# Kernel tuning notes

Measured on AMD Instinct MI355X. Metric: run time of the kernel, lower is better.

The kernel has to match this reference:

```python
import jax, jax.numpy as jnp
import numpy as np

B, S, IN_DIM, D, H, L, C = 8, 1024, 256, 1024, 16, 6, 10
DK = D // H
EPS = 1e-5


def setup_inputs() -> dict:
    key = jax.random.key(0)
    ks = iter(jax.random.split(key, 64))
    n = lambda shape, s=0.02: jax.random.normal(next(ks), shape, dtype=jnp.float32) * s
    inp = {
        'x': jax.random.normal(next(ks), (B, S, IN_DIM), dtype=jnp.float32),
        'emb_w': n((IN_DIM, D)), 'emb_b': jnp.zeros((D,), jnp.float32),
        'Wq': n((L, D, D)), 'bq': jnp.zeros((L, D), jnp.float32),
        'Wk': n((L, D, D)), 'bk': jnp.zeros((L, D), jnp.float32),
        'Wv': n((L, D, D)), 'bv': jnp.zeros((L, D), jnp.float32),
        'Wo': n((L, D, D)), 'bo': jnp.zeros((L, D), jnp.float32),
        'W1': n((L, D, 4 * D)), 'b1': jnp.zeros((L, 4 * D), jnp.float32),
        'W2': n((L, 4 * D, D)), 'b2': jnp.zeros((L, D), jnp.float32),
        'ln1_s': jnp.ones((L, D), jnp.float32), 'ln1_b': jnp.zeros((L, D), jnp.float32),
        'ln2_s': jnp.ones((L, D), jnp.float32), 'ln2_b': jnp.zeros((L, D), jnp.float32),
        'fc_w': n((D, C)), 'fc_b': jnp.zeros((C,), jnp.float32),
    }
    return inp


def _pos_encoding_rows(n_rows):
    # Faithful to the torch module: pe is [max_len,1,D]; pe[:x.size(0)] picks the
    # first `batch` positions and broadcasts over the sequence dim.
    pos = jnp.arange(n_rows, dtype=jnp.float32)[:, None]
    div = jnp.exp(jnp.arange(0, D, 2, dtype=jnp.float32) * (-np.log(10000.0) / D))
    pe = jnp.zeros((n_rows, D), jnp.float32)
    pe = pe.at[:, 0::2].set(jnp.sin(pos * div)).at[:, 1::2].set(jnp.cos(pos * div))
    return pe


def _layer_norm(x, scale, bias):
    mu = jnp.mean(x, axis=-1, keepdims=True)
    var = jnp.mean(jnp.square(x - mu), axis=-1, keepdims=True)
    return (x - mu) * jax.lax.rsqrt(var + EPS) * scale + bias


def reference(x, emb_w, emb_b, Wq, bq, Wk, bk, Wv, bv, Wo, bo,
              W1, b1, W2, b2, ln1_s, ln1_b, ln2_s, ln2_b, fc_w, fc_b):
    h = x @ emb_w + emb_b                              # [B,S,D]
    h = h + _pos_encoding_rows(B)[:, None, :]          # broadcast pe[:B] over seq
    scale = 1.0 / np.sqrt(DK)
    for i in range(L):
        def heads(y, W, b):
            return (y @ W + b).reshape(B, S, H, DK).transpose(0, 2, 1, 3)  # bhsd
        q = heads(h, Wq[i], bq[i])
        k = heads(h, Wk[i], bk[i])
        v = heads(h, Wv[i], bv[i])
        scores = jnp.einsum('bhqd,bhkd->bhqk', q, k) * scale
        p = jax.nn.softmax(scores, axis=-1)
        o = jnp.einsum('bhqk,bhkd->bhqd', p, v)
        o = o.transpose(0, 2, 1, 3).reshape(B, S, D)
        attn_out = o @ Wo[i] + bo[i]
        h = _layer_norm(h + attn_out, ln1_s[i], ln1_b[i])
        ff = jax.nn.relu(h @ W1[i] + b1[i]) @ W2[i] + b2[i]
        h = _layer_norm(h + ff, ln2_s[i], ln2_b[i])
    pooled = jnp.mean(h, axis=1)                       # [B,D]
    return pooled @ fc_w + fc_b                        # [B,C]
```

## Files before the change

kernel.cpp:

```cpp
#include <hip/hip_runtime.h>
#include <stdint.h>

#define B_   8
#define S_   1024
#define IND  256
#define D_   1024
#define H_   16
#define DKH  64
#define L_   6
#define FF   4096
#define NTOK (B_*S_)

typedef __bf16 bf16;
typedef __attribute__((ext_vector_type(4))) float  f32x4;
typedef __attribute__((ext_vector_type(8))) __bf16 bf16x8;
typedef __attribute__((ext_vector_type(4))) __bf16 bf16x4;
typedef __attribute__((ext_vector_type(2))) __bf16 bf16x2;

#define AS1 __attribute__((address_space(1)))
#define AS3 __attribute__((address_space(3)))

__device__ __forceinline__ void gload16(const void* g, void* l) {
  __builtin_amdgcn_global_load_lds((AS1 void*)(const_cast<void*>(g)), (AS3 void*)l, 16, 0, 0);
}

__global__ __launch_bounds__(256)
void k_trans(const float* __restrict__ in, bf16* __restrict__ out,
             int K, int N, long inStride, long outStride) {
  __shared__ float t[32][33];
  const float* inp = in + (long)blockIdx.z * inStride;
  bf16* outp = out + (long)blockIdx.z * outStride;
  const int n0 = blockIdx.x * 32, k0 = blockIdx.y * 32;
  const int tx = threadIdx.x & 31, ty = threadIdx.x >> 5;
  #pragma unroll
  for (int j = 0; j < 32; j += 8)
    t[ty + j][tx] = inp[(long)(k0 + ty + j) * N + n0 + tx];
  __syncthreads();
  #pragma unroll
  for (int j = 0; j < 32; j += 8)
    outp[(long)(n0 + ty + j) * K + k0 + tx] = (bf16)t[tx][ty + j];
}

__global__ __launch_bounds__(256)
void k_f2b(const float* __restrict__ in, bf16* __restrict__ out) {
  const long i = ((long)blockIdx.x * 256 + threadIdx.x) * 4;
  f32x4 v = *(const f32x4*)(in + i);
  bf16x4 o;
  #pragma unroll
  for (int j = 0; j < 4; ++j) o[j] = (bf16)v[j];
  *(bf16x4*)(out + i) = o;
}

__global__ __launch_bounds__(256)
void k_pe(float* __restrict__ pe) {
  const int i = blockIdx.x * 256 + threadIdx.x;
  const int b = i >> 10, d = i & 1023;
  const float k2 = (float)(d & ~1);
  const float dv = __expf(k2 * (-9.210340371976184f / (float)D_));
  const float a = (float)b * dv;
  pe[i] = (d & 1) ? cosf(a) : sinf(a);
}

__global__ __launch_bounds__(256)
void k_packb(const float* __restrict__ bq, const float* __restrict__ bk,
             const float* __restrict__ bv, float* __restrict__ out) {
  const int i = blockIdx.x * 256 + threadIdx.x;
  const int l = i / 3072, j = i % 3072;
  const float* src = (j < 1024) ? bq : ((j < 2048) ? bk : bv);
  out[i] = src[l * 1024 + (j & 1023)];
}

template<int EPI>
__global__ __launch_bounds__(256)
void k_gemm(const bf16* __restrict__ A, const bf16* __restrict__ Bt,
            const float* __restrict__ bias,
            void* __restrict__ out0, void* __restrict__ out1,
            const float* __restrict__ pe,
            int M, int N, int K) {
  __shared__ __align__(16) bf16 sA[128 * 32];
  __shared__ __align__(16) bf16 sB[128 * 32];
  const int tid = threadIdx.x;
  const int lane = tid & 63, wv = tid >> 6;
  const int bx = blockIdx.x, by = blockIdx.y;
  const int wm = wv >> 1, wn = wv & 1;
  const int lg = lane >> 4, lc = lane & 15;
  const long arow0 = (long)by * 128;
  const long brow0 = (long)bx * 128;
  const int c0 = (wv * 2 + 0) * 64 + lane;
  const int c1 = (wv * 2 + 1) * 64 + lane;
  const int r0 = c0 >> 2, s0 = c0 & 3;
  const int r1 = c1 >> 2, s1 = c1 & 3;
  bf16* ldsA0 = sA + (wv * 2 + 0) * 512;
  bf16* ldsA1 = sA + (wv * 2 + 1) * 512;
  bf16* ldsB0 = sB + (wv * 2 + 0) * 512;
  bf16* ldsB1 = sB + (wv * 2 + 1) * 512;
  const bf16* Ab = A + arow0 * K;
  const bf16* Bb = Bt + brow0 * K;
  f32x4 acc[4][4] = {};
  const int kT = K >> 5;
  for (int kt = 0; kt < kT; ++kt) {
    const int k0 = kt << 5;
    gload16(Ab + (long)r0 * K + k0 + s0 * 8, ldsA0);
    gload16(Ab + (long)r1 * K + k0 + s1 * 8, ldsA1);
    gload16(Bb + (long)r0 * K + k0 + s0 * 8, ldsB0);
    gload16(Bb + (long)r1 * K + k0 + s1 * 8, ldsB1);
    __syncthreads();
    bf16x8 af[4], bfr[4];
    #pragma unroll
    for (int mr = 0; mr < 4; ++mr)
      af[mr] = *(const bf16x8*)(sA + (wm * 64 + mr * 16 + lc) * 32 + lg * 8);
    #pragma unroll
    for (int nc = 0; nc < 4; ++nc)
      bfr[nc] = *(const bf16x8*)(sB + (wn * 64 + nc * 16 + lc) * 32 + lg * 8);
    #pragma unroll
    for (int mr = 0; mr < 4; ++mr)
      #pragma unroll
      for (int nc = 0; nc < 4; ++nc)
        acc[mr][nc] = __builtin_amdgcn_mfma_f32_16x16x32_bf16(af[mr], bfr[nc], acc[mr][nc], 0, 0, 0);
    __syncthreads();
  }
  #pragma unroll
  for (int mr = 0; mr < 4; ++mr) {
    const int row0 = by * 128 + wm * 64 + mr * 16 + lg * 4;
    #pragma unroll
    for (int nc = 0; nc < 4; ++nc) {
      const int col = bx * 128 + wn * 64 + nc * 16 + lc;
      const float bvv = bias[col];
      #pragma unroll
      for (int r = 0; r < 4; ++r) {
        float v = acc[mr][nc][r] + bvv;
        const long rr = row0 + r;
        if constexpr (EPI == 0) {
          ((bf16*)out0)[rr * N + col] = (bf16)v;
        } else {
          const long bb = rr >> 10;
          v += pe[bb * D_ + col];
          ((float*)out0)[rr * N + col] = v;
          ((bf16*)out1)[rr * N + col] = (bf16)v;
        }
      }
    }
  }
}

template<int EPI, int SPLIT>
__global__ __launch_bounds__(512, 2)
void k_gemm256(const bf16* __restrict__ A, const bf16* __restrict__ Bt,
               const float* __restrict__ bias,
               void* __restrict__ out0, void* __restrict__ out1,
               float* __restrict__ pout,
               int M, int N, int K) {
  __shared__ __align__(16) bf16 lds[65536];
  const int tid = threadIdx.x;
  const int lane = tid & 63, wv = tid >> 6;
  const int wm = wv >> 2, wn = wv & 3;
  const int lg = lane >> 4, lc = lane & 15;
  const int tileRow = blockIdx.y * 256, tileCol = blockIdx.x * 256;
  const int kHalf = SPLIT ? (K >> 1) : K;
  const long kOff = SPLIT ? (long)blockIdx.z * kHalf : 0;
  const bf16* Abase = A + (long)tileRow * K + kOff;
  const bf16* Bbase = Bt + (long)tileCol * K + kOff;
  const long laneOff = (long)lc * K + lg * 8;
  f32x4 acc[8][4] = {};
  const int NT = kHalf >> 6;
  const int NI = NT >> 1;

  auto stA = [&](int t, int h, int bb) {
    const int rg = h * 16 + wv * 2;
    const int mb = rg >> 1;
    const bf16* s = Abase + (long)(mb * 16) * K + t * 64 + laneOff;
    bf16* d = lds + bb * 32768 + rg * 512;
    gload16(s, d);
    gload16(s + 32, d + 512);
  };
  auto stB = [&](int t, int h, int bb) {
    const int rg = h * 16 + wv * 2;
    const int mb = rg >> 1;
    const bf16* s = Bbase + (long)(mb * 16) * K + t * 64 + laneOff;
    bf16* d = lds + bb * 32768 + 16384 + rg * 512;
    gload16(s, d);
    gload16(s + 32, d + 512);
  };

  bf16x8 aF[8];
  bf16x8 bF0[4], bF1[4];

#define LDA(BB, MH) do { _Pragma("unroll") for (int m = 0; m < 4; ++m) \
    _Pragma("unroll") for (int kk = 0; kk < 2; ++kk) \
      aF[m*2+kk] = *(const bf16x8*)(lds + (BB)*32768 + ((wm*8 + (MH)*4 + m)*2 + kk)*512 + lane*8); \
  } while(0)
#define LDB(BB, NH, DST) do { _Pragma("unroll") for (int n = 0; n < 2; ++n) \
    _Pragma("unroll") for (int kk = 0; kk < 2; ++kk) \
      DST[n*2+kk] = *(const bf16x8*)(lds + (BB)*32768 + 16384 + ((wn*4 + (NH)*2 + n)*2 + kk)*512 + lane*8); \
  } while(0)
#define MM(MH, NH, BSRC, VM) do { \
    if ((VM) == 1) asm volatile("s_waitcnt vmcnt(8)" ::: "memory"); \
    if ((VM) == 2) asm volatile("s_waitcnt vmcnt(0)" ::: "memory"); \
    __builtin_amdgcn_s_barrier(); \
    __builtin_amdgcn_s_setprio(1); \
    _Pragma("unroll") for (int m = 0; m < 4; ++m) \
      _Pragma("unroll") for (int n = 0; n < 2; ++n) { \
        acc[(MH)*4+m][(NH)*2+n] = __builtin_amdgcn_mfma_f32_16x16x32_bf16(aF[m*2+0], BSRC[n*2+0], acc[(MH)*4+m][(NH)*2+n], 0, 0, 0); \
        acc[(MH)*4+m][(NH)*2+n] = __builtin_amdgcn_mfma_f32_16x16x32_bf16(aF[m*2+1], BSRC[n*2+1], acc[(MH)*4+m][(NH)*2+n], 0, 0, 0); \
      } \
    __builtin_amdgcn_s_setprio(0); \
    __builtin_amdgcn_s_barrier(); \
  } while(0)

  stA(0, 0, 0); stB(0, 0, 0); stA(0, 1, 0); stB(0, 1, 0);
  stA(1, 0, 1); stB(1, 0, 1); stA(1, 1, 1); stB(1, 1, 1);
  asm volatile("s_waitcnt vmcnt(8)" ::: "memory");
  __builtin_amdgcn_s_barrier();

  for (int i = 0; i < NI - 1; ++i) {
    const int t2 = 2 * i + 2, t3 = 2 * i + 3;
    LDA(0, 0); LDB(0, 0, bF0);                    MM(0, 0, bF0, 0);
    LDB(0, 1, bF1);            stA(t2, 0, 0);     MM(0, 1, bF1, 0);
    LDA(0, 1);                 stB(t2, 0, 0);     MM(1, 0, bF0, 0);
                  stA(t2, 1, 0); stB(t2, 1, 0);   MM(1, 1, bF1, 1);
    LDA(1, 0); LDB(1, 0, bF0);                    MM(0, 0, bF0, 0);
    LDB(1, 1, bF1);            stA(t3, 0, 1);     MM(0, 1, bF1, 0);
    LDA(1, 1);                 stB(t3, 0, 1);     MM(1, 0, bF0, 0);
                  stA(t3, 1, 1); stB(t3, 1, 1);   MM(1, 1, bF1, 1);
  }
  {
    LDA(0, 0); LDB(0, 0, bF0);                    MM(0, 0, bF0, 0);
    LDB(0, 1, bF1);                               MM(0, 1, bF1, 0);
    LDA(0, 1);                                    MM(1, 0, bF0, 0);
                                                  MM(1, 1, bF1, 2);
    LDA(1, 0); LDB(1, 0, bF0);                    MM(0, 0, bF0, 0);
    LDB(1, 1, bF1);                               MM(0, 1, bF1, 0);
    LDA(1, 1);                                    MM(1, 0, bF0, 0);
                                                  MM(1, 1, bF1, 0);
  }
#undef LDA
#undef LDB
#undef MM

  const bool wpart = SPLIT && (blockIdx.z == 1);
  #pragma unroll
  for (int mr = 0; mr < 8; ++mr) {
    const int row0 = tileRow + wm * 128 + mr * 16 + lg * 4;
    #pragma unroll
    for (int nr = 0; nr < 4; ++nr) {
      const int col = tileCol + wn * 64 + nr * 16 + lc;
      const float bvv = bias[col];
      if (wpart) {
        #pragma unroll
        for (int r = 0; r < 4; ++r)
          pout[(long)(row0 + r) * N + col] = acc[mr][nr][r];
      } else if constexpr (EPI == 2) {
        const int which = col >> 10;
        const int hh = (col & 1023) >> 6;
        const int dk = col & 63;
        const long bb = row0 >> 10;
        const int sr = row0 & 1023;
        if (which == 2) {
          bf16x4 pk;
          #pragma unroll
          for (int r = 0; r < 4; ++r) pk[r] = (bf16)(acc[mr][nr][r] + bvv);
          *(bf16x4*)((bf16*)out1 + ((bb * H_ + hh) * (long)DKH + dk) * S_ + sr) = pk;
        } else {
          #pragma unroll
          for (int r = 0; r < 4; ++r) {
            float v = acc[mr][nr][r] + bvv;
            if (which == 0) v *= 0.125f;
            ((bf16*)out0)[(long)which * NTOK * D_ + ((bb * H_ + hh) * (long)S_ + sr + r) * DKH + dk] = (bf16)v;
          }
        }
      } else {
        #pragma unroll
        for (int r = 0; r < 4; ++r) {
          float v = acc[mr][nr][r] + bvv;
          const long rr = row0 + r;
          if constexpr (EPI == 1) v = fmaxf(v, 0.f);
          ((bf16*)out0)[rr * N + col] = (bf16)v;
        }
      }
    }
  }
}

__global__ __launch_bounds__(256)
void k_flash(const bf16* __restrict__ qg, const bf16* __restrict__ kgl,
             const bf16* __restrict__ vtg, bf16* __restrict__ og) {
  __shared__ __align__(16) bf16 sK[64 * 64];
  __shared__ __align__(16) bf16 sV[64 * 64];
  __shared__ __align__(16) bf16 sP[4 * 16 * 64];
  const int tid = threadIdx.x, lane = tid & 63, wv = tid >> 6;
  const int lg = lane >> 4, lc = lane & 15;
  const int bh = blockIdx.y, qt = blockIdx.x;
  const long base = (long)bh * S_ * DKH;
  const bf16* qb = qg + base;
  const bf16* kb = kgl + base;
  const bf16* vb = vtg + base;
  const int qrow = qt * 64 + wv * 16 + lc;
  const bf16x8 qf0 = *(const bf16x8*)(qb + (long)qrow * DKH + lg * 8);
  const bf16x8 qf1 = *(const bf16x8*)(qb + (long)qrow * DKH + 32 + lg * 8);
  float mrun = -3e38f, lrun = 0.f;
  f32x4 oacc[4] = {};
  bf16* sPw = sP + wv * (16 * 64);
  const int swzP = (lc & 7) << 4;
  const int c0 = wv * 128 + lane, c1 = c0 + 64;
  const int r0 = c0 >> 3, sl0 = (c0 & 7) ^ (r0 & 7);
  const int r1 = c1 >> 3, sl1 = (c1 & 7) ^ (r1 & 7);
  bf16* dst0 = sK + c0 * 8 - lane * 8;
  bf16* dst1 = sK + c1 * 8 - lane * 8;
  bf16* dstV0 = sV + c0 * 8 - lane * 8;
  bf16* dstV1 = sV + c1 * 8 - lane * 8;
  for (int kt = 0; kt < S_ / 64; ++kt) {
    const int gk = kt * 64;
    gload16(kb + (long)(gk + r0) * DKH + sl0 * 8, dst0);
    gload16(kb + (long)(gk + r1) * DKH + sl1 * 8, dst1);
    gload16(vb + (long)r0 * S_ + gk + sl0 * 8, dstV0);
    gload16(vb + (long)r1 * S_ + gk + sl1 * 8, dstV1);
    __syncthreads();
    f32x4 sacc[4] = {};
    #pragma unroll
    for (int nc = 0; nc < 4; ++nc) {
      const int kr = nc * 16 + lc;
      bf16x8 k0 = *(const bf16x8*)((char*)sK + kr * 128 + (((0 + lg) ^ (kr & 7)) << 4));
      bf16x8 k1 = *(const bf16x8*)((char*)sK + kr * 128 + (((4 + lg) ^ (kr & 7)) << 4));
      sacc[nc] = __builtin_amdgcn_mfma_f32_16x16x32_bf16(k0, qf0, sacc[nc], 0, 0, 0);
      sacc[nc] = __builtin_amdgcn_mfma_f32_16x16x32_bf16(k1, qf1, sacc[nc], 0, 0, 0);
    }
    float pm = sacc[0][0];
    #pragma unroll
    for (int nc = 0; nc < 4; ++nc)
      #pragma unroll
      for (int r = 0; r < 4; ++r) pm = fmaxf(pm, sacc[nc][r]);
    pm = fmaxf(pm, __shfl_xor(pm, 16));
    pm = fmaxf(pm, __shfl_xor(pm, 32));
    const float mnew = fmaxf(mrun, pm);
    const float fac = __expf(mrun - mnew);
    float ps = 0.f;
    #pragma unroll
    for (int nc = 0; nc < 4; ++nc)
      #pragma unroll
      for (int r = 0; r < 4; ++r) {
        const float p = __expf(sacc[nc][r] - mnew);
        sacc[nc][r] = p;
        ps += p;
      }
    ps += __shfl_xor(ps, 16);
    ps += __shfl_xor(ps, 32);
    lrun = lrun * fac + ps;
    mrun = mnew;
    #pragma unroll
    for (int nc = 0; nc < 4; ++nc)
      #pragma unroll
      for (int rp = 0; rp < 2; ++rp) {
        bf16x2 t;
        t[0] = (bf16)sacc[nc][rp * 2 + 0];
        t[1] = (bf16)sacc[nc][rp * 2 + 1];
        *(bf16x2*)((char*)sPw + lc * 128 + ((nc * 32 + lg * 8 + rp * 4) ^ swzP)) = t;
      }
    asm volatile("s_waitcnt lgkmcnt(0)" ::: "memory");
    __builtin_amdgcn_sched_barrier(0);
    float fr[4];
    #pragma unroll
    for (int r = 0; r < 4; ++r) fr[r] = __shfl(fac, lg * 4 + r);
    #pragma unroll
    for (int nc = 0; nc < 4; ++nc)
      #pragma unroll
      for (int r = 0; r < 4; ++r) oacc[nc][r] *= fr[r];
    #pragma unroll
    for (int m = 0; m < 2; ++m) {
      const bf16x8 pf = *(const bf16x8*)((char*)sPw + lc * 128 + ((m * 64 + lg * 16) ^ swzP));
      #pragma unroll
      for (int nc = 0; nc < 4; ++nc) {
        const int vr = nc * 16 + lc;
        bf16x8 vf = *(const bf16x8*)((char*)sV + vr * 128 + (((m * 4 + lg) ^ (vr & 7)) << 4));
        oacc[nc] = __builtin_amdgcn_mfma_f32_16x16x32_bf16(pf, vf, oacc[nc], 0, 0, 0);
      }
    }
    __syncthreads();
  }
  const int b = bh >> 4, h = bh & 15;
  const float linv = 1.f / lrun;
  #pragma unroll
  for (int r = 0; r < 4; ++r) {
    const float inv = __shfl(linv, lg * 4 + r);
    const int s = qt * 64 + wv * 16 + lg * 4 + r;
    const long obase = (((long)b * S_ + s) * H_ + h) * DKH;
    #pragma unroll
    for (int nc = 0; nc < 4; ++nc)
      og[obase + nc * 16 + lc] = (bf16)(oacc[nc][r] * inv);
  }
}

template<int TWO>
__global__ __launch_bounds__(256)
void k_addln(const float* __restrict__ hin, const bf16* __restrict__ dlt,
             const float* __restrict__ p1,
             const float* __restrict__ sc, const float* __restrict__ bi,
             float* __restrict__ hout, bf16* __restrict__ hbout) {
  const int row = blockIdx.x, t = threadIdx.x;
  const long off = (long)row * D_ + t * 4;
  f32x4 hv = *(const f32x4*)(hin + off);
  bf16x4 dv = *(const bf16x4*)(dlt + off);
  f32x4 pv;
  if constexpr (TWO) pv = *(const f32x4*)(p1 + off);
  f32x4 x;
  float s = 0.f, ss = 0.f;
  #pragma unroll
  for (int j = 0; j < 4; ++j) {
    x[j] = hv[j] + (float)dv[j];
    if constexpr (TWO) x[j] += pv[j];
    s += x[j]; ss += x[j] * x[j];
  }
  #pragma unroll
  for (int m = 1; m < 64; m <<= 1) { s += __shfl_xor(s, m); ss += __shfl_xor(ss, m); }
  __shared__ float red[8];
  const int w = t >> 6, ln = t & 63;
  if (ln == 0) { red[w] = s; red[4 + w] = ss; }
  __syncthreads();
  s = red[0] + red[1] + red[2] + red[3];
  ss = red[4] + red[5] + red[6] + red[7];
  const float mu = s * (1.f / D_);
  const float rstd = rsqrtf(ss * (1.f / D_) - mu * mu + 1e-5f);
  f32x4 scv = *(const f32x4*)(sc + t * 4);
  f32x4 biv = *(const f32x4*)(bi + t * 4);
  f32x4 y; bf16x4 yb;
  #pragma unroll
  for (int j = 0; j < 4; ++j) { y[j] = (x[j] - mu) * rstd * scv[j] + biv[j]; yb[j] = (bf16)y[j]; }
  *(f32x4*)(hout + off) = y;
  *(bf16x4*)(hbout + off) = yb;
}

__global__ __launch_bounds__(256)
void k_pool1(const float* __restrict__ h, float* __restrict__ part) {
  const int i = blockIdx.x * 256 + threadIdx.x;
  const int b = i >> 10, d = i & 1023;
  const int s0 = blockIdx.y * 128;
  float s = 0.f;
  for (int t = 0; t < 128; ++t) s += h[((long)b * S_ + s0 + t) * D_ + d];
  part[(long)blockIdx.y * NTOK + i] = s;
}

__global__ __launch_bounds__(256)
void k_pool2(const float* __restrict__ part, float* __restrict__ pooled) {
  const int i = blockIdx.x * 256 + threadIdx.x;
  float s = 0.f;
  #pragma unroll
  for (int j = 0; j < 8; ++j) s += part[(long)j * NTOK + i];
  pooled[i] = s * (1.f / S_);
}

__global__ __launch_bounds__(64)
void k_fc(const float* __restrict__ pooled, const float* __restrict__ fw,
          const float* __restrict__ fb, float* __restrict__ out) {
  const int b = blockIdx.x / 10, c = blockIdx.x % 10;
  const int lane = threadIdx.x;
  float s = 0.f;
  for (int d = lane; d < D_; d += 64) s += pooled[b * D_ + d] * fw[d * 10 + c];
  #pragma unroll
  for (int m = 1; m < 64; m <<= 1) s += __shfl_xor(s, m);
  if (lane == 0) out[b * 10 + c] = s + fb[c];
}

extern "C" void kernel_launch(void* const* d_in, const int* in_sizes, int n_in,
                              void* d_out, int out_size, void* d_ws, size_t ws_size,
                              hipStream_t stream) {
  const float* x     = (const float*)d_in[0];
  const float* emb_w = (const float*)d_in[1];
  const float* emb_b = (const float*)d_in[2];
  const float* Wq    = (const float*)d_in[3];
  const float* bq    = (const float*)d_in[4];
  const float* Wk    = (const float*)d_in[5];
  const float* bk    = (const float*)d_in[6];
  const float* Wv    = (const float*)d_in[7];
  const float* bv    = (const float*)d_in[8];
  const float* Wo    = (const float*)d_in[9];
  const float* bo    = (const float*)d_in[10];
  const float* W1    = (const float*)d_in[11];
  const float* b1    = (const float*)d_in[12];
  const float* W2    = (const float*)d_in[13];
  const float* b2    = (const float*)d_in[14];
  const float* ln1s  = (const float*)d_in[15];
  const float* ln1b  = (const float*)d_in[16];
  const float* ln2s  = (const float*)d_in[17];
  const float* ln2b  = (const float*)d_in[18];
  const float* fcw   = (const float*)d_in[19];
  const float* fcb   = (const float*)d_in[20];

  char* w = (char*)d_ws;
  size_t off = 0;
  auto alloc = [&](size_t bytes) -> char* {
    char* p = w + off;
    off += (bytes + 255) & ~(size_t)255;
    return p;
  };
  bf16*  x_bf  = (bf16*) alloc((size_t)NTOK * IND * 2);
  bf16*  embT  = (bf16*) alloc((size_t)D_ * IND * 2);
  bf16*  qkvT  = (bf16*) alloc((size_t)L_ * 3 * D_ * D_ * 2);
  bf16*  woT   = (bf16*) alloc((size_t)L_ * D_ * D_ * 2);
  bf16*  w1T   = (bf16*) alloc((size_t)L_ * FF * D_ * 2);
  bf16*  w2T   = (bf16*) alloc((size_t)L_ * D_ * FF * 2);
  float* qkvB  = (float*)alloc((size_t)L_ * 3 * D_ * 4);
  float* pe    = (float*)alloc((size_t)B_ * D_ * 4);
  float* h_f   = (float*)alloc((size_t)NTOK * D_ * 4);
  bf16*  h_b   = (bf16*) alloc((size_t)NTOK * D_ * 2);
  bf16*  delta = (bf16*) alloc((size_t)NTOK * D_ * 2);
  float* pooled= (float*)alloc((size_t)B_ * D_ * 4);
  float* part  = (float*)alloc((size_t)8 * NTOK * 4);
  bf16*  scratch = (bf16*)alloc((size_t)NTOK * FF * 2);
  bf16* qb  = scratch;
  bf16* kb  = scratch + (size_t)NTOK * D_;
  bf16* vTb = scratch + (size_t)2 * NTOK * D_;
  bf16* ob  = scratch + (size_t)3 * NTOK * D_;
  bf16* ffn1 = scratch;
  float* p1 = (float*)alloc((size_t)NTOK * D_ * 4);
  const bool canSplit = (off <= ws_size);
  (void)in_sizes; (void)n_in; (void)out_size;

  k_f2b<<<dim3(NTOK * IND / 1024), dim3(256), 0, stream>>>(x, x_bf);
  k_trans<<<dim3(D_ / 32, IND / 32, 1), dim3(256), 0, stream>>>(emb_w, embT, IND, D_, 0, 0);
  k_trans<<<dim3(32, 32, L_), dim3(256), 0, stream>>>(Wq, qkvT,               D_, D_, (long)D_ * D_, (long)3 * D_ * D_);
  k_trans<<<dim3(32, 32, L_), dim3(256), 0, stream>>>(Wk, qkvT + D_ * D_,     D_, D_, (long)D_ * D_, (long)3 * D_ * D_);
  k_trans<<<dim3(32, 32, L_), dim3(256), 0, stream>>>(Wv, qkvT + 2 * D_ * D_, D_, D_, (long)D_ * D_, (long)3 * D_ * D_);
  k_trans<<<dim3(32, 32, L_), dim3(256), 0, stream>>>(Wo, woT, D_, D_, (long)D_ * D_, (long)D_ * D_);
  k_trans<<<dim3(FF / 32, 32, L_), dim3(256), 0, stream>>>(W1, w1T, D_, FF, (long)D_ * FF, (long)FF * D_);
  k_trans<<<dim3(32, FF / 32, L_), dim3(256), 0, stream>>>(W2, w2T, FF, D_, (long)FF * D_, (long)D_ * FF);
  k_pe<<<dim3(B_ * D_ / 256), dim3(256), 0, stream>>>(pe);
  k_packb<<<dim3(L_ * 3 * D_ / 256), dim3(256), 0, stream>>>(bq, bk, bv, qkvB);

  k_gemm<3><<<dim3(D_ / 128, NTOK / 128), dim3(256), 0, stream>>>(
      x_bf, embT, emb_b, h_f, h_b, pe, NTOK, D_, IND);

  for (int l = 0; l < L_; ++l) {
    k_gemm256<2, 0><<<dim3(3 * D_ / 256, NTOK / 256), dim3(512), 0, stream>>>(
        h_b, qkvT + (size_t)l * 3 * D_ * D_, qkvB + l * 3 * D_,
        qb, vTb, nullptr, NTOK, 3 * D_, D_);
    k_flash<<<dim3(S_ / 64, B_ * H_), dim3(256), 0, stream>>>(qb, kb, vTb, ob);
    if (canSplit) {
      k_gemm256<0, 1><<<dim3(D_ / 256, NTOK / 256, 2), dim3(512), 0, stream>>>(
          ob, woT + (size_t)l * D_ * D_, bo + l * D_,
          delta, nullptr, p1, NTOK, D_, D_);
      k_addln<1><<<dim3(NTOK), dim3(256), 0, stream>>>(h_f, delta, p1, ln1s + l * D_, ln1b + l * D_, h_f, h_b);
    } else {
      k_gemm256<0, 0><<<dim3(D_ / 256, NTOK / 256), dim3(512), 0, stream>>>(
          ob, woT + (size_t)l * D_ * D_, bo + l * D_,
          delta, nullptr, nullptr, NTOK, D_, D_);
      k_addln<0><<<dim3(NTOK), dim3(256), 0, stream>>>(h_f, delta, nullptr, ln1s + l * D_, ln1b + l * D_, h_f, h_b);
    }
    k_gemm256<1, 0><<<dim3(FF / 256, NTOK / 256), dim3(512), 0, stream>>>(
        h_b, w1T + (size_t)l * FF * D_, b1 + l * FF,
        ffn1, nullptr, nullptr, NTOK, FF, D_);
    if (canSplit) {
      k_gemm256<0, 1><<<dim3(D_ / 256, NTOK / 256, 2), dim3(512), 0, stream>>>(
          ffn1, w2T + (size_t)l * D_ * FF, b2 + l * D_,
          delta, nullptr, p1, NTOK, D_, FF);
      k_addln<1><<<dim3(NTOK), dim3(256), 0, stream>>>(h_f, delta, p1, ln2s + l * D_, ln2b + l * D_, h_f, h_b);
    } else {
      k_gemm256<0, 0><<<dim3(D_ / 256, NTOK / 256), dim3(512), 0, stream>>>(
          ffn1, w2T + (size_t)l * D_ * FF, b2 + l * D_,
          delta, nullptr, nullptr, NTOK, D_, FF);
      k_addln<0><<<dim3(NTOK), dim3(256), 0, stream>>>(h_f, delta, nullptr, ln2s + l * D_, ln2b + l * D_, h_f, h_b);
    }
  }

  k_pool1<<<dim3(NTOK / 256, 8), dim3(256), 0, stream>>>(h_f, part);
  k_pool2<<<dim3(NTOK / 256), dim3(256), 0, stream>>>(part, pooled);
  k_fc<<<dim3(B_ * 10), dim3(64), 0, stream>>>(pooled, fcw, fcb, (float*)d_out);
}
```

Baseline: 2.389 ms.

## Remap workgroups across XCDs, trim GEMM barriers, and keep split-K partials in fp32

Adds an XCD-aware block-id remap to the 256x256 GEMM and the flash-attention kernel, so neighbouring tiles land on the same XCD and share its L2. The GEMM pipeline now uses one barrier per MFMA phase instead of two, and waits on vmcnt only at buffer switches. Split-K now writes both halves as fp32 partials, and the bias is added in the add+LayerNorm kernel instead of through a bf16 delta. This removes one rounding step and some barrier stalls, at the cost of an extra fp32 buffer and more partial-sum memory traffic.

After: 2.358 ms. Within noise of the previous version (-1.3%).

```diff
diff --git a/kernel.cpp b/kernel.cpp
--- a/kernel.cpp
+++ b/kernel.cpp
@@ -148,14 +148,20 @@
 void k_gemm256(const bf16* __restrict__ A, const bf16* __restrict__ Bt,
                const float* __restrict__ bias,
                void* __restrict__ out0, void* __restrict__ out1,
-               float* __restrict__ pout,
+               float* __restrict__ pout0, float* __restrict__ pout1,
                int M, int N, int K) {
   __shared__ __align__(16) bf16 lds[65536];
   const int tid = threadIdx.x;
   const int lane = tid & 63, wv = tid >> 6;
   const int wm = wv >> 2, wn = wv & 3;
   const int lg = lane >> 4, lc = lane & 15;
-  const int tileRow = blockIdx.y * 256, tileCol = blockIdx.x * 256;
+  const int gx = gridDim.x;
+  const int nwg = gx * gridDim.y;
+  int bid = blockIdx.x + blockIdx.y * gx;
+  const int cpx = nwg >> 3;
+  bid = (bid & 7) * cpx + (bid >> 3);
+  const int bxs = bid % gx, bys = bid / gx;
+  const int tileRow = bys * 256, tileCol = bxs * 256;
   const int kHalf = SPLIT ? (K >> 1) : K;
   const long kOff = SPLIT ? (long)blockIdx.z * kHalf : 0;
   const bf16* Abase = A + (long)tileRow * K + kOff;
@@ -193,10 +199,7 @@
     _Pragma("unroll") for (int kk = 0; kk < 2; ++kk) \
       DST[n*2+kk] = *(const bf16x8*)(lds + (BB)*32768 + 16384 + ((wn*4 + (NH)*2 + n)*2 + kk)*512 + lane*8); \
   } while(0)
-#define MM(MH, NH, BSRC, VM) do { \
-    if ((VM) == 1) asm volatile("s_waitcnt vmcnt(8)" ::: "memory"); \
-    if ((VM) == 2) asm volatile("s_waitcnt vmcnt(0)" ::: "memory"); \
-    __builtin_amdgcn_s_barrier(); \
+#define MMA(MH, NH, BSRC) do { \
     __builtin_amdgcn_s_setprio(1); \
     _Pragma("unroll") for (int m = 0; m < 4; ++m) \
       _Pragma("unroll") for (int n = 0; n < 2; ++n) { \
@@ -204,52 +207,55 @@
         acc[(MH)*4+m][(NH)*2+n] = __builtin_amdgcn_mfma_f32_16x16x32_bf16(aF[m*2+1], BSRC[n*2+1], acc[(MH)*4+m][(NH)*2+n], 0, 0, 0); \
       } \
     __builtin_amdgcn_s_setprio(0); \
-    __builtin_amdgcn_s_barrier(); \
   } while(0)
+#define VM8 asm volatile("s_waitcnt vmcnt(8)" ::: "memory")
+#define VM0 asm volatile("s_waitcnt vmcnt(0)" ::: "memory")
+#define BAR __builtin_amdgcn_s_barrier()
 
   stA(0, 0, 0); stB(0, 0, 0); stA(0, 1, 0); stB(0, 1, 0);
   stA(1, 0, 1); stB(1, 0, 1); stA(1, 1, 1); stB(1, 1, 1);
-  asm volatile("s_waitcnt vmcnt(8)" ::: "memory");
-  __builtin_amdgcn_s_barrier();
 
   for (int i = 0; i < NI - 1; ++i) {
     const int t2 = 2 * i + 2, t3 = 2 * i + 3;
-    LDA(0, 0); LDB(0, 0, bF0);                    MM(0, 0, bF0, 0);
-    LDB(0, 1, bF1);            stA(t2, 0, 0);     MM(0, 1, bF1, 0);
-    LDA(0, 1);                 stB(t2, 0, 0);     MM(1, 0, bF0, 0);
-                  stA(t2, 1, 0); stB(t2, 1, 0);   MM(1, 1, bF1, 1);
-    LDA(1, 0); LDB(1, 0, bF0);                    MM(0, 0, bF0, 0);
-    LDB(1, 1, bF1);            stA(t3, 0, 1);     MM(0, 1, bF1, 0);
-    LDA(1, 1);                 stB(t3, 0, 1);     MM(1, 0, bF0, 0);
-                  stA(t3, 1, 1); stB(t3, 1, 1);   MM(1, 1, bF1, 1);
+    VM8; BAR; LDA(0, 0); LDB(0, 0, bF0);                    MMA(0, 0, bF0);
+         BAR; LDB(0, 1, bF1); stA(t2, 0, 0);                MMA(0, 1, bF1);
+         BAR; LDA(0, 1);      stB(t2, 0, 0);                MMA(1, 0, bF0);
+         BAR;                 stA(t2, 1, 0); stB(t2, 1, 0); MMA(1, 1, bF1);
+    VM8; BAR; LDA(1, 0); LDB(1, 0, bF0);                    MMA(0, 0, bF0);
+         BAR; LDB(1, 1, bF1); stA(t3, 0, 1);                MMA(0, 1, bF1);
+         BAR; LDA(1, 1);      stB(t3, 0, 1);                MMA(1, 0, bF0);
+         BAR;                 stA(t3, 1, 1); stB(t3, 1, 1); MMA(1, 1, bF1);
   }
   {
-    LDA(0, 0); LDB(0, 0, bF0);                    MM(0, 0, bF0, 0);
-    LDB(0, 1, bF1);                               MM(0, 1, bF1, 0);
-    LDA(0, 1);                                    MM(1, 0, bF0, 0);
-                                                  MM(1, 1, bF1, 2);
-    LDA(1, 0); LDB(1, 0, bF0);                    MM(0, 0, bF0, 0);
-    LDB(1, 1, bF1);                               MM(0, 1, bF1, 0);
-    LDA(1, 1);                                    MM(1, 0, bF0, 0);
-                                                  MM(1, 1, bF1, 0);
+    VM8; BAR; LDA(0, 0); LDB(0, 0, bF0); MMA(0, 0, bF0);
+         BAR; LDB(0, 1, bF1);            MMA(0, 1, bF1);
+         BAR; LDA(0, 1);                 MMA(1, 0, bF0);
+         BAR;                            MMA(1, 1, bF1);
+    VM0; BAR; LDA(1, 0); LDB(1, 0, bF0); MMA(0, 0, bF0);
+         BAR; LDB(1, 1, bF1);            MMA(0, 1, bF1);
+         BAR; LDA(1, 1);                 MMA(1, 0, bF0);
+         BAR;                            MMA(1, 1, bF1);
   }
 #undef LDA
 #undef LDB
-#undef MM
-
-  const bool wpart = SPLIT && (blockIdx.z == 1);
+#undef MMA
+#undef VM8
+#undef VM0
+#undef BAR
+
   #pragma unroll
   for (int mr = 0; mr < 8; ++mr) {
     const int row0 = tileRow + wm * 128 + mr * 16 + lg * 4;
     #pragma unroll
     for (int nr = 0; nr < 4; ++nr) {
       const int col = tileCol + wn * 64 + nr * 16 + lc;
-      const float bvv = bias[col];
-      if (wpart) {
+      if constexpr (SPLIT) {
+        float* po = blockIdx.z ? pout1 : pout0;
         #pragma unroll
         for (int r = 0; r < 4; ++r)
-          pout[(long)(row0 + r) * N + col] = acc[mr][nr][r];
+          po[(long)(row0 + r) * N + col] = acc[mr][nr][r];
       } else if constexpr (EPI == 2) {
+        const float bvv = bias[col];
         const int which = col >> 10;
         const int hh = (col & 1023) >> 6;
         const int dk = col & 63;
@@ -269,6 +275,7 @@
           }
         }
       } else {
+        const float bvv = bias[col];
         #pragma unroll
         for (int r = 0; r < 4; ++r) {
           float v = acc[mr][nr][r] + bvv;
@@ -289,7 +296,9 @@
   __shared__ __align__(16) bf16 sP[4 * 16 * 64];
   const int tid = threadIdx.x, lane = tid & 63, wv = tid >> 6;
   const int lg = lane >> 4, lc = lane & 15;
-  const int bh = blockIdx.y, qt = blockIdx.x;
+  int bid = blockIdx.x + blockIdx.y * 16;
+  bid = (bid & 7) * 256 + (bid >> 3);
+  const int qt = bid & 15, bh = bid >> 4;
   const long base = (long)bh * S_ * DKH;
   const bf16* qb = qg + base;
   const bf16* kb = kgl + base;
@@ -392,23 +401,28 @@
 template<int TWO>
 __global__ __launch_bounds__(256)
 void k_addln(const float* __restrict__ hin, const bf16* __restrict__ dlt,
-             const float* __restrict__ p1,
+             const float* __restrict__ p0, const float* __restrict__ p1,
+             const float* __restrict__ gb,
              const float* __restrict__ sc, const float* __restrict__ bi,
              float* __restrict__ hout, bf16* __restrict__ hbout) {
   const int row = blockIdx.x, t = threadIdx.x;
   const long off = (long)row * D_ + t * 4;
   f32x4 hv = *(const f32x4*)(hin + off);
-  bf16x4 dv = *(const bf16x4*)(dlt + off);
-  f32x4 pv;
-  if constexpr (TWO) pv = *(const f32x4*)(p1 + off);
   f32x4 x;
+  if constexpr (TWO) {
+    f32x4 a = *(const f32x4*)(p0 + off);
+    f32x4 b = *(const f32x4*)(p1 + off);
+    f32x4 g = *(const f32x4*)(gb + t * 4);
+    #pragma unroll
+    for (int j = 0; j < 4; ++j) x[j] = hv[j] + a[j] + b[j] + g[j];
+  } else {
+    bf16x4 dv = *(const bf16x4*)(dlt + off);
+    #pragma unroll
+    for (int j = 0; j < 4; ++j) x[j] = hv[j] + (float)dv[j];
+  }
   float s = 0.f, ss = 0.f;
   #pragma unroll
-  for (int j = 0; j < 4; ++j) {
-    x[j] = hv[j] + (float)dv[j];
-    if constexpr (TWO) x[j] += pv[j];
-    s += x[j]; ss += x[j] * x[j];
-  }
+  for (int j = 0; j < 4; ++j) { s += x[j]; ss += x[j] * x[j]; }
   #pragma unroll
   for (int m = 1; m < 64; m <<= 1) { s += __shfl_xor(s, m); ss += __shfl_xor(ss, m); }
   __shared__ float red[8];
@@ -510,6 +524,7 @@
   bf16* vTb = scratch + (size_t)2 * NTOK * D_;
   bf16* ob  = scratch + (size_t)3 * NTOK * D_;
   bf16* ffn1 = scratch;
+  float* p0 = (float*)alloc((size_t)NTOK * D_ * 4);
   float* p1 = (float*)alloc((size_t)NTOK * D_ * 4);
   const bool canSplit = (off <= ws_size);
   (void)in_sizes; (void)n_in; (void)out_size;
@@ -531,32 +546,36 @@
   for (int l = 0; l < L_; ++l) {
     k_gemm256<2, 0><<<dim3(3 * D_ / 256, NTOK / 256), dim3(512), 0, stream>>>(
         h_b, qkvT + (size_t)l * 3 * D_ * D_, qkvB + l * 3 * D_,
-        qb, vTb, nullptr, NTOK, 3 * D_, D_);
+        qb, vTb, nullptr, nullptr, NTOK, 3 * D_, D_);
     k_flash<<<dim3(S_ / 64, B_ * H_), dim3(256), 0, stream>>>(qb, kb, vTb, ob);
     if (canSplit) {
       k_gemm256<0, 1><<<dim3(D_ / 256, NTOK / 256, 2), dim3(512), 0, stream>>>(
-          ob, woT + (size_t)l * D_ * D_, bo + l * D_,
-          delta, nullptr, p1, NTOK, D_, D_);
-      k_addln<1><<<dim3(NTOK), dim3(256), 0, stream>>>(h_f, delta, p1, ln1s + l * D_, ln1b + l * D_, h_f, h_b);
+          ob, woT + (size_t)l * D_ * D_, nullptr,
+          nullptr, nullptr, p0, p1, NTOK, D_, D_);
+      k_addln<1><<<dim3(NTOK), dim3(256), 0, stream>>>(
+          h_f, nullptr, p0, p1, bo + l * D_, ln1s + l * D_, ln1b + l * D_, h_f, h_b);
     } else {
       k_gemm256<0, 0><<<dim3(D_ / 256, NTOK / 256), dim3(512), 0, stream>>>(
           ob, woT + (size_t)l * D_ * D_, bo + l * D_,
-          delta, nullptr, nullptr, NTOK, D_, D_);
-      k_addln<0><<<dim3(NTOK), dim3(256), 0, stream>>>(h_f, delta, nullptr, ln1s + l * D_, ln1b + l * D_, h_f, h_b);
+          delta, nullptr, nullptr, nullptr, NTOK, D_, D_);
+      k_addln<0><<<dim3(NTOK), dim3(256), 0, stream>>>(
+          h_f, delta, nullptr, nullptr, nullptr, ln1s + l * D_, ln1b + l * D_, h_f, h_b);
     }
     k_gemm256<1, 0><<<dim3(FF / 256, NTOK / 256), dim3(512), 0, stream>>>(
         h_b, w1T + (size_t)l * FF * D_, b1 + l * FF,
-        ffn1, nullptr, nullptr, NTOK, FF, D_);
+        ffn1, nullptr, nullptr, nullptr, NTOK, FF, D_);
     if (canSplit) {
       k_gemm256<0, 1><<<dim3(D_ / 256, NTOK / 256, 2), dim3(512), 0, stream>>>(
-          ffn1, w2T + (size_t)l * D_ * FF, b2 + l * D_,
-          delta, nullptr, p1, NTOK, D_, FF);
-      k_addln<1><<<dim3(NTOK), dim3(256), 0, stream>>>(h_f, delta, p1, ln2s + l * D_, ln2b + l * D_, h_f, h_b);
+          ffn1, w2T + (size_t)l * D_ * FF, nullptr,
+          nullptr, nullptr, p0, p1, NTOK, D_, FF);
+      k_addln<1><<<dim3(NTOK), dim3(256), 0, stream>>>(
+          h_f, nullptr, p0, p1, b2 + l * D_, ln2s + l * D_, ln2b + l * D_, h_f, h_b);
     } else {
       k_gemm256<0, 0><<<dim3(D_ / 256, NTOK / 256), dim3(512), 0, stream>>>(
           ffn1, w2T + (size_t)l * D_ * FF, b2 + l * D_,
-          delta, nullptr, nullptr, NTOK, D_, FF);
-      k_addln<0><<<dim3(NTOK), dim3(256), 0, stream>>>(h_f, delta, nullptr, ln2s + l * D_, ln2b + l * D_, h_f, h_b);
+          delta, nullptr, nullptr, nullptr, NTOK, D_, FF);
+      k_addln<0><<<dim3(NTOK), dim3(256), 0, stream>>>(
+          h_f, delta, nullptr, nullptr, nullptr, ln2s + l * D_, ln2b + l * D_, h_f, h_b);
     }
   }
 
```
